# Performance work log

Measured on AMD Instinct MI355X. Metric: run time of the kernel, lower is better.

The kernel has to match this reference:

```python
import jax, jax.numpy as jnp
import numpy as np


def _run_stacked_lstm(x, init_hc, params):
    """x: [B,T,E]; init_hc: tuple of (h,c) per layer; params: tuple of (W,U,b) per layer.
    Keras LSTMCell gate order: i, f, g(candidate), o; sigmoid recurrent act, tanh act."""
    def step(carry, xt):
        inp = xt
        new = []
        for (h, c), (W, U, b) in zip(carry, params):
            z = inp @ W + h @ U + b                      # [B, 4*units]
            i, f, g, o = jnp.split(z, 4, axis=-1)
            c2 = jax.nn.sigmoid(f) * c + jax.nn.sigmoid(i) * jnp.tanh(g)
            h2 = jax.nn.sigmoid(o) * jnp.tanh(c2)
            new.append((h2, c2))
            inp = h2                                     # feed to next layer
        return tuple(new), inp
    carry, ys = jax.lax.scan(step, init_hc, jnp.swapaxes(x, 0, 1))
    return jnp.swapaxes(ys, 0, 1), carry                 # [B,T,units], final states


def setup_inputs() -> dict:
    key = jax.random.key(0)
    ks = jax.random.split(key, 20)
    B, T, V, E, H, L = 16, 64, 32000, 512, 512, 2
    s = 0.02
    inp = {
        'ids_1': jax.random.randint(ks[0], (B, T), 0, V),
        'ids_2': jax.random.randint(ks[1], (B, T), 0, V),
        'init_state': jax.random.normal(ks[2], (L, B, H), jnp.float32),
        'emb': jax.random.normal(ks[3], (V, E), jnp.float32) * s,
        'W1_0': jax.random.normal(ks[4], (E, 4 * H), jnp.float32) * s,
        'U1_0': jax.random.normal(ks[5], (H, 4 * H), jnp.float32) * s,
        'b1_0': jnp.zeros((4 * H,), jnp.float32),
        'W1_1': jax.random.normal(ks[6], (H, 4 * H), jnp.float32) * s,
        'U1_1': jax.random.normal(ks[7], (H, 4 * H), jnp.float32) * s,
        'b1_1': jnp.zeros((4 * H,), jnp.float32),
        'W2_0': jax.random.normal(ks[8], (E, 8 * H), jnp.float32) * s,
        'U2_0': jax.random.normal(ks[9], (2 * H, 8 * H), jnp.float32) * s,
        'b2_0': jnp.zeros((8 * H,), jnp.float32),
        'W2_1': jax.random.normal(ks[10], (2 * H, 8 * H), jnp.float32) * s,
        'U2_1': jax.random.normal(ks[11], (2 * H, 8 * H), jnp.float32) * s,
        'b2_1': jnp.zeros((8 * H,), jnp.float32),
        'Wp1': jax.random.normal(ks[12], (H, V), jnp.float32) * s,
        'bp1': jnp.zeros((V,), jnp.float32),
        'Wp2': jax.random.normal(ks[13], (2 * H, V), jnp.float32) * s,
        'bp2': jnp.zeros((V,), jnp.float32),
    }
    return inp


def reference(ids_1, ids_2, init_state, emb,
              W1_0, U1_0, b1_0, W1_1, U1_1, b1_1,
              W2_0, U2_0, b2_0, W2_1, U2_1, b2_1,
              Wp1, bp1, Wp2, bp2):
    L = init_state.shape[0]
    e1 = emb[ids_1]                                       # [B,T,E]
    e2 = emb[ids_2]
    # RNN1: initial (h,c) both set to init_state per layer
    init1 = tuple((init_state[l], init_state[l]) for l in range(L))
    p1 = ((W1_0, U1_0, b1_0), (W1_1, U1_1, b1_1))
    out1, st1 = _run_stacked_lstm(e1, init1, p1)
    logits1 = out1 @ Wp1 + bp1                            # [B,T,V]
    # RNN2: initial h = concat(init, h1_final), c = concat(init, c1_final)
    init2 = tuple((jnp.concatenate([init_state[l], st1[l][0]], axis=1),
                   jnp.concatenate([init_state[l], st1[l][1]], axis=1))
                  for l in range(L))
    p2 = ((W2_0, U2_0, b2_0), (W2_1, U2_1, b2_1))
    out2, _ = _run_stacked_lstm(e2, init2, p2)
    logits2 = out2 @ Wp2 + bp2                            # [B,T,V]
    return (logits1, logits2)
```

## Files before the change

### kernel.cpp

```cpp
#include <hip/hip_runtime.h>
#include <hip/hip_bf16.h>

#define B_ 16
#define T_ 64
#define E_ 512
#define H_ 512
#define V_ 32000

typedef __attribute__((ext_vector_type(4))) float f32x4;
typedef __attribute__((ext_vector_type(8))) short s16x8;

__device__ __forceinline__ float sigm(float x){ return 1.0f/(1.0f + __expf(-x)); }

__device__ __forceinline__ unsigned short f2bf(float x){
  unsigned int u = __float_as_uint(x);
  return (unsigned short)((u + 0x7FFFu + ((u>>16)&1u)) >> 16);
}

__device__ __forceinline__ unsigned load_coh(const unsigned* p){
  unsigned v;
  asm volatile("global_load_dword %0, %1, off sc0 sc1\n\ts_waitcnt vmcnt(0)"
               : "=v"(v) : "v"(p) : "memory");
  return v;
}
__device__ __forceinline__ void store_coh16(unsigned short* p, unsigned v){
  asm volatile("global_store_short %0, %1, off sc0 sc1" :: "v"(p), "v"(v) : "memory");
}
__device__ __forceinline__ void store_cohf(float* p, float v){
  asm volatile("global_store_dword %0, %1, off sc0 sc1" :: "v"(p), "v"(v) : "memory");
}
__device__ __forceinline__ void store_cohu(unsigned* p, unsigned v){
  asm volatile("global_store_dword %0, %1, off sc0 sc1" :: "v"(p), "v"(v) : "memory");
}

__device__ __forceinline__ void gbar3(unsigned* barb, unsigned bi1, int nblk,
                                      bool det, int myblk){
  asm volatile("s_waitcnt vmcnt(0)" ::: "memory");
  __syncthreads();
  const int tid = threadIdx.x;
  if(tid == 0) store_cohu(barb + (size_t)myblk*16, bi1);
  if(det){
    if(tid < nblk){
      const unsigned* fp = barb + (size_t)tid*16;
      while(load_coh(fp) < bi1) __builtin_amdgcn_s_sleep(1);
    }
    __syncthreads();
    if(tid < 8) store_cohu(barb + 4096 + (size_t)tid*16, bi1);
  } else {
    if(tid == 0){
      const unsigned* gp = barb + 4096 + (size_t)(myblk & 7)*16;
      while(load_coh(gp) < bi1) __builtin_amdgcn_s_sleep(1);
    }
  }
  __syncthreads();
}

__global__ void k_barinit(unsigned* bar){
  int i = blockIdx.x*256 + threadIdx.x;
  if(i < 16384) bar[i] = 0u;
}

__global__ void k_gather(const int* __restrict__ ids, const float* __restrict__ emb,
                         unsigned short* __restrict__ out){
  const int row = blockIdx.x;
  const int id  = ids[row];
  float4 v = *(const float4*)(emb + (size_t)id*E_ + threadIdx.x*4);
  ushort4 o;
  o.x = f2bf(v.x); o.y = f2bf(v.y); o.z = f2bf(v.z); o.w = f2bf(v.w);
  *(ushort4*)(out + (size_t)row*E_ + threadIdx.x*4) = o;
}

__device__ __forceinline__ void tcvt_dev(const float* __restrict__ in,
    unsigned short* __restrict__ out, int N, int Hp, int Kfull, int koff, int swz,
    int bx, int by, float (*tile)[33]){
  const int n0 = bx*32, k0 = by*32;
  const int x = threadIdx.x & 31, y = threadIdx.x >> 5;
  __syncthreads();
  #pragma unroll
  for(int i=0;i<4;i++){
    int k = y + i*8;
    tile[k][x] = in[(size_t)(k0+k)*N + n0 + x];
  }
  __syncthreads();
  #pragma unroll
  for(int i=0;i<4;i++){
    int nl = y + i*8;
    int n  = n0 + nl;
    int p  = Hp ? ((n % Hp)*4 + n / Hp) : n;
    int kk = koff + k0 + x;
    size_t idx;
    if(swz){
      int k2 = kk*2;
      int slot = ((k2>>4)&7) ^ (p&7);
      idx = (size_t)p*Kfull + (((k2 & ~127) | (slot<<4) | (k2 & 15)) >> 1);
    } else {
      idx = (size_t)p*Kfull + kk;
    }
    out[idx] = f2bf(tile[x][nl]);
  }
}

__global__ __launch_bounds__(256)
void k_tcvt(const float* __restrict__ in, unsigned short* __restrict__ out,
            int N, int Hp, int Kfull, int koff, int swz){
  __shared__ float tile[32][33];
  tcvt_dev(in, out, N, Hp, Kfull, koff, swz, blockIdx.x, blockIdx.y, tile);
}

__device__ __forceinline__ void tcvtw_dev(const float* __restrict__ in,
    unsigned short* __restrict__ out, int N, int K, int bx, int by,
    float (*tile)[257]){
  const int tid = threadIdx.x;
  const int n0 = bx*256, k0 = by*32;
  const int row = tid >> 3, nc = (tid & 7)*32;
  __syncthreads();
  #pragma unroll
  for(int j=0;j<8;j++){
    float4 v = *(const float4*)(in + (size_t)(k0+row)*N + n0 + nc + j*4);
    *(float4*)&tile[row][nc + j*4] = v;
  }
  __syncthreads();
  __align__(16) unsigned short vals[32];
  #pragma unroll
  for(int k=0;k<32;k++) vals[k] = f2bf(tile[k][tid]);
  unsigned short* op = out + (size_t)(n0+tid)*K + k0;
  #pragma unroll
  for(int j=0;j<4;j++)
    *(uint4*)(op + j*8) = *(const uint4*)&vals[j*8];
}

__global__ void k_bpack(const float* __restrict__ b, float* __restrict__ out, int H, int N){
  int p = blockIdx.x*256 + threadIdx.x;
  if(p < N) out[p] = b[(p&3)*H + (p>>2)];
}

__global__ void k_init1(const float* __restrict__ init_state,
                        unsigned short* h0i, float* c0i, unsigned short* h1i, float* c1i){
  int i = blockIdx.x*256 + threadIdx.x;
  if(i >= B_*H_) return;
  float v0 = init_state[i];
  float v1 = init_state[B_*H_ + i];
  h0i[i] = f2bf(v0); c0i[i] = v0;
  h1i[i] = f2bf(v1); c1i[i] = v1;
}

__global__ void k_init2(const float* __restrict__ init_state,
                        const unsigned short* __restrict__ h0seq1,
                        const unsigned short* __restrict__ h1seq1,
                        const float* __restrict__ c0f1, const float* __restrict__ c1f1,
                        unsigned short* h20i, unsigned short* h21i,
                        float* c20i, float* c21i){
  const int l = blockIdx.y;
  int i = blockIdx.x*256 + threadIdx.x;
  if(i >= B_*2*H_) return;
  const int r = i >> 10, j = i & 1023;
  unsigned short* ho = l ? h21i : h20i;
  float* co = l ? c21i : c20i;
  if(j < H_){
    float v = init_state[(size_t)l*B_*H_ + r*H_ + j];
    ho[i] = f2bf(v); co[i] = v;
  } else {
    const unsigned short* hs = l ? h1seq1 : h0seq1;
    const float* cf = l ? c1f1 : c0f1;
    ho[i] = hs[(size_t)((T_-1)*B_ + r)*H_ + (j - H_)];
    co[i] = cf[r*H_ + (j - H_)];
  }
}

__device__ __forceinline__ void mm_tile(const unsigned short* __restrict__ A,
    const unsigned short* __restrict__ Bt, const float* __restrict__ bias,
    float* __restrict__ C, int N, int K, int bm, int bn,
    unsigned short* As, unsigned short* Bs, int remap){
  const int tid = threadIdx.x;
  const int lane = tid & 63, w = tid >> 6;
  const int wm = (w>>1)*64, wn = (w&1)*64;
  const int l15 = lane & 15, kg = lane >> 4;
  f32x4 acc[4][4] = {};
  for(int k0=0; k0<K; k0+=64){
    __syncthreads();
    #pragma unroll
    for(int ch=0; ch<4; ch++){
      int off = ch*4096 + tid*16;
      int row = off >> 7;
      int s   = ((off >> 4) & 7) ^ (row & 7);
      __builtin_amdgcn_global_load_lds(
        (const __attribute__((address_space(1))) unsigned int*)(A + (size_t)(bm+row)*K + k0 + s*8),
        (__attribute__((address_space(3))) unsigned int*)((char*)As + off), 16, 0, 0);
    }
    #pragma unroll
    for(int ch=0; ch<4; ch++){
      int off = ch*4096 + tid*16;
      int row = off >> 7;
      int s   = ((off >> 4) & 7) ^ (row & 7);
      __builtin_amdgcn_global_load_lds(
        (const __attribute__((address_space(1))) unsigned int*)(Bt + (size_t)(bn+row)*K + k0 + s*8),
        (__attribute__((address_space(3))) unsigned int*)((char*)Bs + off), 16, 0, 0);
    }
    __syncthreads();
    #pragma unroll
    for(int q=0;q<2;q++){
      s16x8 af[4], bf[4];
      #pragma unroll
      for(int mt=0;mt<4;mt++){
        int row = wm + mt*16 + l15;
        int s = (q*4 + kg) ^ (row & 7);
        af[mt] = *(const s16x8*)(As + row*64 + s*8);
      }
      #pragma unroll
      for(int nt=0;nt<4;nt++){
        int row = wn + nt*16 + l15;
        int s = (q*4 + kg) ^ (row & 7);
        bf[nt] = *(const s16x8*)(Bs + row*64 + s*8);
      }
      #pragma unroll
      for(int mt=0;mt<4;mt++)
        #pragma unroll
        for(int nt=0;nt<4;nt++)
          acc[mt][nt] = __builtin_amdgcn_mfma_f32_16x16x32_bf16(af[mt], bf[nt], acc[mt][nt], 0, 0, 0);
    }
  }
  #pragma unroll
  for(int mt=0;mt<4;mt++){
    #pragma unroll
    for(int nt=0;nt<4;nt++){
      int col = bn + wn + nt*16 + l15;
      float bv = bias ? bias[col] : 0.f;
      #pragma unroll
      for(int e=0;e<4;e++){
        int row = bm + wm + mt*16 + kg*4 + e;
        int orow = remap ? ((row & 15)*T_ + (row >> 4)) : row;
        C[(size_t)orow*N + col] = acc[mt][nt][e] + bv;
      }
    }
  }
}

template<int BF32>
__global__ __launch_bounds__(256)
void k_mm(const unsigned short* __restrict__ A, const void* __restrict__ Bsrc,
          const float* __restrict__ bias, float* __restrict__ C,
          int M, int N, int K, int remap, int bm0){
  __shared__ __align__(16) unsigned short As[128*64];
  __shared__ __align__(16) unsigned short Bs[128*64];
  if(!BF32){
    mm_tile(A, (const unsigned short*)Bsrc, bias, C, N, K,
            bm0 + blockIdx.y*128, blockIdx.x*128, As, Bs, remap);
    return;
  }
  const int tid = threadIdx.x;
  const int lane = tid & 63, w = tid >> 6;
  const int wm = (w>>1)*64, wn = (w&1)*64;
  const int bm = bm0 + blockIdx.y*128, bn = blockIdx.x*128;
  const int l15 = lane & 15, kg = lane >> 4;
  f32x4 acc[4][4] = {};
  for(int k0=0; k0<K; k0+=64){
    __syncthreads();
    #pragma unroll
    for(int ch=0; ch<4; ch++){
      int off = ch*4096 + tid*16;
      int row = off >> 7;
      int s   = ((off >> 4) & 7) ^ (row & 7);
      __builtin_amdgcn_global_load_lds(
        (const __attribute__((address_space(1))) unsigned int*)(A + (size_t)(bm+row)*K + k0 + s*8),
        (__attribute__((address_space(3))) unsigned int*)((char*)As + off), 16, 0, 0);
    }
    {
      const float* Bf = (const float*)Bsrc;
      #pragma unroll
      for(int i=0;i<8;i++){
        int kl = (tid>>5) + i*8;
        int nl = (tid&31)*4;
        float4 v = *(const float4*)(Bf + (size_t)(k0+kl)*N + bn + nl);
        int slot = kl >> 3, kb = kl & 7;
        float vv[4] = {v.x, v.y, v.z, v.w};
        #pragma unroll
        for(int jj=0;jj<4;jj++){
          int n = nl + jj;
          Bs[n*64 + ((slot ^ (n&7))*8) + kb] = f2bf(vv[jj]);
        }
      }
    }
    __syncthreads();
    #pragma unroll
    for(int q=0;q<2;q++){
      s16x8 af[4], bf[4];
      #pragma unroll
      for(int mt=0;mt<4;mt++){
        int row = wm + mt*16 + l15;
        int s = (q*4 + kg) ^ (row & 7);
        af[mt] = *(const s16x8*)(As + row*64 + s*8);
      }
      #pragma unroll
      for(int nt=0;nt<4;nt++){
        int row = wn + nt*16 + l15;
        int s = (q*4 + kg) ^ (row & 7);
        bf[nt] = *(const s16x8*)(Bs + row*64 + s*8);
      }
      #pragma unroll
      for(int mt=0;mt<4;mt++)
        #pragma unroll
        for(int nt=0;nt<4;nt++)
          acc[mt][nt] = __builtin_amdgcn_mfma_f32_16x16x32_bf16(af[mt], bf[nt], acc[mt][nt], 0, 0, 0);
    }
  }
  #pragma unroll
  for(int mt=0;mt<4;mt++){
    #pragma unroll
    for(int nt=0;nt<4;nt++){
      int col = bn + wn + nt*16 + l15;
      float bv = bias ? bias[col] : 0.f;
      #pragma unroll
      for(int e=0;e<4;e++){
        int row = bm + wm + mt*16 + kg*4 + e;
        int orow = remap ? ((row & 15)*T_ + (row >> 4)) : row;
        C[(size_t)orow*N + col] = acc[mt][nt][e] + bv;
      }
    }
  }
}

template<int C, int K, int LAYER, int HU, int TB>
__device__ __forceinline__ void rnn_body(
    unsigned short* __restrict__ Uld, float* __restrict__ zp,
    const unsigned short* __restrict__ Uslice,
    const float* __restrict__ xw0, const float* __restrict__ bpk,
    const unsigned short* __restrict__ h0init, const unsigned short* __restrict__ h1init,
    const float* __restrict__ cinit,
    unsigned short* __restrict__ h0seq, unsigned short* __restrict__ h1seq,
    float* __restrict__ cfin, unsigned* bar, int cb, int nblk, bool det, int myblk)
{
  constexpr int KW = K/4, KS = KW/32, FR = C/16, UB = C/4;
  constexpr int K2 = K*2;
  constexpr int ITEMS = 16*UB;
  const int tid = threadIdx.x;
  const int lane = tid & 63, w = tid >> 6;
  const int l15 = lane & 15, kg = lane >> 4;

  constexpr int CP = (C*K2)/4096;
  #pragma unroll
  for(int i=0;i<CP;i++){
    __builtin_amdgcn_global_load_lds(
      (const __attribute__((address_space(1))) unsigned int*)((const char*)Uslice + i*4096 + tid*16),
      (__attribute__((address_space(3))) unsigned int*)((char*)Uld + i*4096 + tid*16), 16, 0, 0);
  }
  const int base_p = cb*C;
  const int base_u = cb*UB;
  float4 bvr = make_float4(0.f,0.f,0.f,0.f);
  int er = 0, eu = 0;
  if(tid < ITEMS){ er = tid / UB; eu = tid - er*UB; bvr = *(const float4*)(bpk + base_p + eu*4); }
  float creg = 0.f;
  unsigned short* hseqW = LAYER ? h1seq : h0seq;

  int cbyte[FR], cx[FR];
  #pragma unroll
  for(int f=0;f<FR;f++){ int c = f*16 + l15; cbyte[f] = c*K2; cx[f] = (c&7)<<4; }

  __syncthreads();

  for(int it = 0; it <= T_; ++it){
    const bool active = LAYER ? (it >= 1) : (it < T_);
    const int t = LAYER ? it-1 : it;
    if(active){
      const unsigned short* asrc;
      if constexpr(LAYER == 0){
        asrc = (t == 0) ? (h0init + l15*HU)
             : (h0seq + ((size_t)(TB ? ((t-1)*B_ + l15) : (l15*T_ + (t-1))))*HU);
      } else {
        if(w < 2){
          asrc = h0seq + ((size_t)(TB ? (t*B_ + l15) : (l15*T_ + t)))*HU;
        } else {
          asrc = ((t == 0) ? (h1init + l15*HU)
               : (h1seq + ((size_t)(TB ? ((t-1)*B_ + l15) : (l15*T_ + (t-1))))*HU)) - HU;
        }
      }
      f32x4 acc[FR];
      #pragma unroll
      for(int f=0;f<FR;f++) acc[f] = (f32x4){0.f,0.f,0.f,0.f};
      #pragma unroll
      for(int s=0;s<KS;s++){
        const int kel = w*KW + s*32 + kg*8;
        s16x8 a = *(const s16x8*)(asrc + kel);
        const int kb  = kel*2;
        const int kch = kb & ~127;
        const int ksl = (kb >> 4) & 7;
        #pragma unroll
        for(int f=0;f<FR;f++){
          const int ad = cbyte[f] + kch + ((ksl<<4) ^ cx[f]);
          s16x8 b = *(const s16x8*)((const char*)Uld + ad);
          acc[f] = __builtin_amdgcn_mfma_f32_16x16x32_bf16(a, b, acc[f], 0, 0, 0);
        }
      }
      #pragma unroll
      for(int f=0;f<FR;f++)
        #pragma unroll
        for(int e=0;e<4;e++)
          zp[(w*16 + kg*4 + e)*68 + f*16 + l15] = acc[f][e];
    }
    __syncthreads();
    if(active && tid < ITEMS){
      float4 z0 = *(const float4*)(zp + (     er)*68 + eu*4);
      float4 z1 = *(const float4*)(zp + (16 + er)*68 + eu*4);
      float4 z2 = *(const float4*)(zp + (32 + er)*68 + eu*4);
      float4 z3 = *(const float4*)(zp + (48 + er)*68 + eu*4);
      float si = z0.x+z1.x+z2.x+z3.x + bvr.x;
      float sf = z0.y+z1.y+z2.y+z3.y + bvr.y;
      float sg = z0.z+z1.z+z2.z+z3.z + bvr.z;
      float so = z0.w+z1.w+z2.w+z3.w + bvr.w;
      if constexpr(LAYER == 0){
        float4 xv = *(const float4*)(xw0 + ((size_t)(er*T_ + t))*(4*HU) + base_p + eu*4);
        si += xv.x; sf += xv.y; sg += xv.z; so += xv.w;
      }
      float cin = (t == 0) ? cinit[er*HU + base_u + eu] : creg;
      float c2 = sigm(sf)*cin + sigm(si)*tanhf(sg);
      float h2 = sigm(so)*tanhf(c2);
      creg = c2;
      size_t hrow = TB ? ((size_t)(t*B_ + er)) : ((size_t)(er*T_ + t));
      store_coh16(&hseqW[hrow*HU + base_u + eu], (unsigned)f2bf(h2));
      if(t == T_-1) store_cohf(&cfin[er*HU + base_u + eu], c2);
    }
    if(it < T_) gbar3(bar, (unsigned)(it+1), nblk, det, myblk);
  }
  asm volatile("s_waitcnt vmcnt(0)" ::: "memory");
  __syncthreads();
  if(tid == 0) store_cohu(bar + (size_t)myblk*16, (unsigned)(T_+1));
}

__global__ __launch_bounds__(256, 1)
void k_rnn1m(const unsigned short* __restrict__ Ut0, const unsigned short* __restrict__ WU1,
    const float* __restrict__ xw0, const float* __restrict__ bpk0, const float* __restrict__ bpk1,
    const unsigned short* __restrict__ h0init, const unsigned short* __restrict__ h1init,
    const float* __restrict__ c0init, const float* __restrict__ c1init,
    unsigned short* __restrict__ h0seq, unsigned short* __restrict__ h1seq,
    float* __restrict__ c0fin, float* __restrict__ c1fin, unsigned* bar,
    const int* __restrict__ ids2, const float* __restrict__ emb, unsigned short* __restrict__ ebuf2,
    const float* __restrict__ b2_0, const float* __restrict__ b2_1,
    float* __restrict__ bpk20, float* __restrict__ bpk21,
    const float* __restrict__ U2_0, unsigned short* __restrict__ ut0_2,
    const float* __restrict__ W2_0, unsigned short* __restrict__ wtmp2,
    const float* __restrict__ W2_1, const float* __restrict__ U2_1, unsigned short* __restrict__ wu1_2,
    const float* __restrict__ Wp1, unsigned short* __restrict__ wpT1,
    const float* __restrict__ Wp2, unsigned short* __restrict__ wpT2,
    const float* __restrict__ bp1, float* __restrict__ out1,
    float* __restrict__ xw2buf, int wide)
{
  constexpr int HU = 512, C0 = 64, C1 = 64;
  constexpr int NB0 = 4*HU/C0;
  constexpr int NRNN = NB0 + 4*HU/C1;
  constexpr int NS = 256 - NRNN;
  __shared__ __align__(16) unsigned short Uld[65536];
  __shared__ __align__(16) float zred[64*68];
  const int blk = blockIdx.x;
  const int tid = threadIdx.x;
  if(blk < NB0){
    rnn_body<C0, HU, 0, HU, 1>(Uld, zred, Ut0 + (size_t)blk*C0*HU, xw0, bpk0,
        h0init, h1init, c0init, h0seq, h1seq, c0fin, bar, blk, NRNN, blk==0, blk);
  } else if(blk < NRNN){
    rnn_body<C1, 2*HU, 1, HU, 1>(Uld, zred, WU1 + (size_t)(blk-NB0)*C1*2*HU, nullptr, bpk1,
        h0init, h1init, c1init, h0seq, h1seq, c1fin, bar, blk-NB0, NRNN, false, blk);
  } else {
    const int q = blk - NRNN;
    float (*tile)[33]   = (float(*)[33])Uld;
    float (*tile2)[257] = (float(*)[257])Uld;
    unsigned short* As = Uld;
    unsigned short* Bs = Uld + 8192;
    volatile int* rdy = (volatile int*)((char*)Uld + 128000);
    const int J0 = 512, J1 = J0+32, J2 = J1+4096, J3 = J2+2048, J4 = J3+4096, J5 = J4+4096;
    const int J6 = J5 + 2000;
    const int J7 = J6 + 4000;
    const int totJ = wide ? J7 : J5;
    for(int j = q; j < totJ; j += NS){
      if(j < J0){
        int row = j*2 + (tid>>7);
        int id = ids2[row];
        float4 v = *(const float4*)(emb + (size_t)id*E_ + (tid&127)*4);
        ushort4 o; o.x=f2bf(v.x); o.y=f2bf(v.y); o.z=f2bf(v.z); o.w=f2bf(v.w);
        *(ushort4*)(ebuf2 + (size_t)row*E_ + (tid&127)*4) = o;
      } else if(j < J1){
        int jj = j - J0;
        const float* b = (jj < 16) ? b2_0 : b2_1;
        float* o = (jj < 16) ? bpk20 : bpk21;
        int p = (jj & 15)*256 + tid;
        o[p] = b[(p&3)*1024 + (p>>2)];
      } else if(j < J2){
        int r = j - J1; tcvt_dev(U2_0, ut0_2, 4096, 1024, 1024, 0, 1, r%128, r/128, tile);
      } else if(j < J3){
        int r = j - J2; tcvt_dev(W2_0, wtmp2, 4096, 1024, 512, 0, 0, r%128, r/128, tile);
      } else if(j < J4){
        int r = j - J3; tcvt_dev(W2_1, wu1_2, 4096, 1024, 2048, 0, 1, r%128, r/128, tile);
      } else if(j < J5){
        int r = j - J4; tcvt_dev(U2_1, wu1_2, 4096, 1024, 2048, 1024, 1, r%128, r/128, tile);
      } else if(j < J6){
        int r = j - J5; tcvtw_dev(Wp1, wpT1, 32000, 512, r%125, r/125, tile2);
      } else {
        int r = j - J6; tcvtw_dev(Wp2, wpT2, 32000, 1024, r%125, r/125, tile2);
      }
    }
    if(!wide) return;
    __syncthreads();
    __threadfence();
    if(tid == 0)
      __hip_atomic_fetch_add(bar + 5120, 1u, __ATOMIC_RELAXED, __HIP_MEMORY_SCOPE_AGENT);
    if(tid == 0){
      while(load_coh(bar + 5120) < (unsigned)NS) __builtin_amdgcn_s_sleep(8);
    }
    __syncthreads();
    if(xw2buf){
      for(int t2 = q; t2 < 256; t2 += NS)
        mm_tile(ebuf2, wtmp2, nullptr, xw2buf, 4096, 512, (t2>>5)*128, (t2&31)*128, As, Bs, 0);
    }
    for(int g = 0; g < 8; ++g){
      const unsigned req = 8u*(unsigned)g + 9u;
      for(;;){
        if(tid == 0) *rdy = 1;
        __syncthreads();
        if(tid < 32){
          if(load_coh(bar + (size_t)(NB0 + tid)*16) < req) *rdy = 0;
        }
        __syncthreads();
        if(*rdy) break;
        __builtin_amdgcn_s_sleep(16);
      }
      for(int n = q; n < 250; n += NS)
        mm_tile(h1seq, wpT1, bp1, out1, V_, 512, g*128, n*128, As, Bs, 1);
    }
  }
}

__global__ __launch_bounds__(256, 1)
void k_rnn2m(const unsigned short* __restrict__ Ut0, const unsigned short* __restrict__ WU1,
    const float* __restrict__ xw0, const float* __restrict__ bpk0, const float* __restrict__ bpk1,
    const unsigned short* __restrict__ h0init, const unsigned short* __restrict__ h1init,
    const float* __restrict__ c0init, const float* __restrict__ c1init,
    unsigned short* __restrict__ h0seq, unsigned short* __restrict__ h1seq,
    float* __restrict__ c0fin, float* __restrict__ c1fin, unsigned* bar,
    const unsigned short* __restrict__ wpT2,
    const float* __restrict__ bp2, float* __restrict__ out2, int wide)
{
  constexpr int HU = 1024, C0 = 64, C1 = 32;
  constexpr int NB0 = 4*HU/C0;
  constexpr int NRNN = NB0 + 4*HU/C1;
  constexpr int NS = 64;
  __shared__ __align__(16) unsigned short Uld[65536];
  __shared__ __align__(16) float zred[64*68];
  const int blk = blockIdx.x;
  const int tid = threadIdx.x;
  if(blk < NB0){
    rnn_body<C0, HU, 0, HU, 1>(Uld, zred, Ut0 + (size_t)blk*C0*HU, xw0, bpk0,
        h0init, h1init, c0init, h0seq, h1seq, c0fin, bar, blk, NRNN, blk==0, blk);
  } else if(blk < NRNN){
    rnn_body<C1, 2*HU, 1, HU, 1>(Uld, zred, WU1 + (size_t)(blk-NB0)*C1*2*HU, nullptr, bpk1,
        h0init, h1init, c1init, h0seq, h1seq, c1fin, bar, blk-NB0, NRNN, false, blk);
  } else if(wide){
    const int q = blk - NRNN;
    unsigned short* As = Uld;
    unsigned short* Bs = Uld + 8192;
    volatile int* rdy = (volatile int*)((char*)Uld + 128000);
    for(int g = 0; g < 6; ++g){
      const unsigned req = 8u*(unsigned)g + 9u;
      for(;;){
        if(tid == 0) *rdy = 1;
        __syncthreads();
        if(tid < 128){
          if(load_coh(bar + (size_t)(NB0 + tid)*16) < req) *rdy = 0;
        }
        __syncthreads();
        if(*rdy) break;
        __builtin_amdgcn_s_sleep(16);
      }
      for(int n = q; n < 250; n += NS)
        mm_tile(h1seq, wpT2, bp2, out2, V_, 1024, g*128, n*128, As, Bs, 1);
    }
  }
}

extern "C" void kernel_launch(void* const* d_in, const int* in_sizes, int n_in,
                              void* d_out, int out_size, void* d_ws, size_t ws_size,
                              hipStream_t stream){
  const int*   ids1 = (const int*)d_in[0];
  const int*   ids2 = (const int*)d_in[1];
  const float* init = (const float*)d_in[2];
  const float* emb  = (const float*)d_in[3];
  const float* W1_0 = (const float*)d_in[4];
  const float* U1_0 = (const float*)d_in[5];
  const float* b1_0 = (const float*)d_in[6];
  const float* W1_1 = (const float*)d_in[7];
  const float* U1_1 = (const float*)d_in[8];
  const float* b1_1 = (const float*)d_in[9];
  const float* W2_0 = (const float*)d_in[10];
  const float* U2_0 = (const float*)d_in[11];
  const float* b2_0 = (const float*)d_in[12];
  const float* W2_1 = (const float*)d_in[13];
  const float* U2_1 = (const float*)d_in[14];
  const float* b2_1 = (const float*)d_in[15];
  const float* Wp1  = (const float*)d_in[16];
  const float* bp1  = (const float*)d_in[17];
  const float* Wp2  = (const float*)d_in[18];
  const float* bp2  = (const float*)d_in[19];
  float* out1 = (float*)d_out;
  float* out2 = out1 + (size_t)B_*T_*V_;

  char* base = (char*)d_ws;
  float*          xw    = (float*)(base);
  unsigned short* ut0_1 = (unsigned short*)(base + (16u<<20));
  unsigned short* wu1_1 = (unsigned short*)(base + (18u<<20));
  unsigned short* ut0_2 = (unsigned short*)(base + (22u<<20));
  unsigned short* wu1_2 = (unsigned short*)(base + (30u<<20));
  unsigned short* wtmp  = (unsigned short*)(base + (46u<<20));
  unsigned short* ebuf  = (unsigned short*)(base + (50u<<20));
  unsigned short* h0s1  = (unsigned short*)(base + (51u<<20));
  unsigned short* h1s1  = (unsigned short*)(base + (52u<<20));
  unsigned short* h0s2  = (unsigned short*)(base + (53u<<20));
  unsigned short* h1s2  = (unsigned short*)(base + (55u<<20));
  char* M = base + (57u<<20);
  unsigned short* h0i1 = (unsigned short*)(M);
  unsigned short* h1i1 = (unsigned short*)(M + 16384);
  float* c0i1 = (float*)(M + 32768);
  float* c1i1 = (float*)(M + 65536);
  unsigned short* h2i0 = (unsigned short*)(M + 98304);
  unsigned short* h2i1 = (unsigned short*)(M + 131072);
  float* c2i0 = (float*)(M + 163840);
  float* c2i1 = (float*)(M + 229376);
  float* c0f1 = (float*)(M + 294912);
  float* c1f1 = (float*)(M + 327680);
  float* c0f2 = (float*)(M + 360448);
  float* c1f2 = (float*)(M + 425984);
  float* bpk10 = (float*)(M + 491520);
  float* bpk11 = (float*)(M + 499712);
  float* bpk20 = (float*)(M + 507904);
  float* bpk21 = (float*)(M + 524288);
  unsigned* bar1 = (unsigned*)(M + 540672);
  unsigned* bar2 = (unsigned*)(M + 540672 + 32768);
  unsigned short* wpT1 = (unsigned short*)(base + (58u<<20));
  unsigned short* wpT2 = (unsigned short*)(base + (90u<<20));
  float*          xw2  = (float*)(base + (153u<<20));
  const size_t NEED_W  = ((size_t)90u<<20) + (size_t)V_*1024*2;
  const size_t NEED_W2 = ((size_t)169u<<20);
  const bool wide  = ws_size >= NEED_W;
  const bool wide2 = ws_size >= NEED_W2;
  float* xw2p = wide2 ? xw2 : xw;

  k_barinit<<<dim3(64), dim3(256), 0, stream>>>(bar1);

  k_init1<<<dim3(32), dim3(256), 0, stream>>>(init, h0i1, c0i1, h1i1, c1i1);
  k_gather<<<dim3(B_*T_), dim3(128), 0, stream>>>(ids1, emb, ebuf);
  k_tcvt<<<dim3(64, 16), dim3(256), 0, stream>>>(U1_0, ut0_1, 2048, 512, 512, 0, 1);
  k_tcvt<<<dim3(64, 16), dim3(256), 0, stream>>>(W1_0, wtmp,  2048, 512, 512, 0, 0);
  k_tcvt<<<dim3(64, 16), dim3(256), 0, stream>>>(W1_1, wu1_1, 2048, 512, 1024, 0, 1);
  k_tcvt<<<dim3(64, 16), dim3(256), 0, stream>>>(U1_1, wu1_1, 2048, 512, 1024, 512, 1);
  k_bpack<<<dim3(8),  dim3(256), 0, stream>>>(b1_0, bpk10, 512, 2048);
  k_bpack<<<dim3(8),  dim3(256), 0, stream>>>(b1_1, bpk11, 512, 2048);
  k_mm<0><<<dim3(16, 8), dim3(256), 0, stream>>>(ebuf, wtmp, nullptr, xw, 1024, 2048, 512, 0, 0);

  k_rnn1m<<<dim3(256), dim3(256), 0, stream>>>(ut0_1, wu1_1, xw, bpk10, bpk11,
      h0i1, h1i1, c0i1, c1i1, h0s1, h1s1, c0f1, c1f1, bar1,
      ids2, emb, ebuf, b2_0, b2_1, bpk20, bpk21,
      U2_0, ut0_2, W2_0, wtmp, W2_1, U2_1, wu1_2,
      Wp1, wpT1, Wp2, wpT2, bp1, out1,
      (wide && wide2) ? xw2 : nullptr, (int)wide);

  if(!wide){
    k_mm<1><<<dim3(250, 8), dim3(256), 0, stream>>>(h1s1, Wp1, bp1, out1, 1024, V_, 512, 1, 0);
  }
  if(!wide || !wide2){
    k_mm<0><<<dim3(32, 8), dim3(256), 0, stream>>>(ebuf, wtmp, nullptr, xw, 1024, 4096, 512, 0, 0);
  }
  k_init2<<<dim3(64, 2), dim3(256), 0, stream>>>(init, h0s1, h1s1, c0f1, c1f1,
                                                 h2i0, h2i1, c2i0, c2i1);

  k_rnn2m<<<dim3(256), dim3(256), 0, stream>>>(ut0_2, wu1_2, xw2p, bpk20, bpk21,
      h2i0, h2i1, c2i0, c2i1, h0s2, h1s2, c0f2, c1f2, bar2,
      wpT2, bp2, out2, (int)wide);

  if(wide){
    k_mm<0><<<dim3(250, 2), dim3(256), 0, stream>>>(h1s2, wpT2, bp2, out2, 1024, V_, 1024, 1, 768);
  } else {
    k_mm<1><<<dim3(250, 8), dim3(256), 0, stream>>>(h1s2, Wp2, bp2, out2, 1024, V_, 1024, 1, 0);
  }
}
```

Before: 1.029 ms.

## Remove overlapped projection from RNN2 kernel and run full projection afterwards

Drops the 64 extra blocks in the second RNN kernel that computed the vocab projection for the first 768 rows while the recurrence ran, leaving a 192-block recurrence-only kernel. The full 1024-row projection for logits2 is now done by a separate matmul launch afterwards. This removes the polling and contention of the projection blocks against the latency-bound recurrence, but gives up the overlap, so most of the projection work now sits on the critical path.

```diff
diff --git a/kernel.cpp b/kernel.cpp
--- a/kernel.cpp
+++ b/kernel.cpp
@@ -526,51 +526,28 @@
   }
 }
 
+template<int HU, int C0, int C1>
 __global__ __launch_bounds__(256, 1)
-void k_rnn2m(const unsigned short* __restrict__ Ut0, const unsigned short* __restrict__ WU1,
-    const float* __restrict__ xw0, const float* __restrict__ bpk0, const float* __restrict__ bpk1,
-    const unsigned short* __restrict__ h0init, const unsigned short* __restrict__ h1init,
-    const float* __restrict__ c0init, const float* __restrict__ c1init,
-    unsigned short* __restrict__ h0seq, unsigned short* __restrict__ h1seq,
-    float* __restrict__ c0fin, float* __restrict__ c1fin, unsigned* bar,
-    const unsigned short* __restrict__ wpT2,
-    const float* __restrict__ bp2, float* __restrict__ out2, int wide)
+void k_rnn(const unsigned short* __restrict__ Ut0, const unsigned short* __restrict__ WU1,
+           const float* __restrict__ xw0, const float* __restrict__ bpk0, const float* __restrict__ bpk1,
+           const unsigned short* __restrict__ h0init, const unsigned short* __restrict__ h1init,
+           const float* __restrict__ c0init, const float* __restrict__ c1init,
+           unsigned short* __restrict__ h0seq, unsigned short* __restrict__ h1seq,
+           float* __restrict__ c0fin, float* __restrict__ c1fin, unsigned* bar)
 {
-  constexpr int HU = 1024, C0 = 64, C1 = 32;
   constexpr int NB0 = 4*HU/C0;
-  constexpr int NRNN = NB0 + 4*HU/C1;
-  constexpr int NS = 64;
-  __shared__ __align__(16) unsigned short Uld[65536];
+  constexpr int UMAXE = (C0*HU > C1*2*HU) ? C0*HU : C1*2*HU;
+  __shared__ __align__(16) unsigned short Uld[UMAXE];
   __shared__ __align__(16) float zred[64*68];
+  const int nblk = gridDim.x;
+  const bool det = (blockIdx.x == 0);
   const int blk = blockIdx.x;
-  const int tid = threadIdx.x;
-  if(blk < NB0){
+  if(blk < NB0)
     rnn_body<C0, HU, 0, HU, 1>(Uld, zred, Ut0 + (size_t)blk*C0*HU, xw0, bpk0,
-        h0init, h1init, c0init, h0seq, h1seq, c0fin, bar, blk, NRNN, blk==0, blk);
-  } else if(blk < NRNN){
+                               h0init, h1init, c0init, h0seq, h1seq, c0fin, bar, blk, nblk, det, blk);
+  else
     rnn_body<C1, 2*HU, 1, HU, 1>(Uld, zred, WU1 + (size_t)(blk-NB0)*C1*2*HU, nullptr, bpk1,
-        h0init, h1init, c1init, h0seq, h1seq, c1fin, bar, blk-NB0, NRNN, false, blk);
-  } else if(wide){
-    const int q = blk - NRNN;
-    unsigned short* As = Uld;
-    unsigned short* Bs = Uld + 8192;
-    volatile int* rdy = (volatile int*)((char*)Uld + 128000);
-    for(int g = 0; g < 6; ++g){
-      const unsigned req = 8u*(unsigned)g + 9u;
-      for(;;){
-        if(tid == 0) *rdy = 1;
-        __syncthreads();
-        if(tid < 128){
-          if(load_coh(bar + (size_t)(NB0 + tid)*16) < req) *rdy = 0;
-        }
-        __syncthreads();
-        if(*rdy) break;
-        __builtin_amdgcn_s_sleep(16);
-      }
-      for(int n = q; n < 250; n += NS)
-        mm_tile(h1seq, wpT2, bp2, out2, V_, 1024, g*128, n*128, As, Bs, 1);
-    }
-  }
+                               h0init, h1init, c1init, h0seq, h1seq, c1fin, bar, blk-NB0, nblk, det, blk);
 }
 
 extern "C" void kernel_launch(void* const* d_in, const int* in_sizes, int n_in,
@@ -637,7 +614,7 @@
   const size_t NEED_W2 = ((size_t)169u<<20);
   const bool wide  = ws_size >= NEED_W;
   const bool wide2 = ws_size >= NEED_W2;
-  float* xw2p = wide2 ? xw2 : xw;
+  float* xw2p = (wide && wide2) ? xw2 : xw;
 
   k_barinit<<<dim3(64), dim3(256), 0, stream>>>(bar1);
 
@@ -667,12 +644,11 @@
   k_init2<<<dim3(64, 2), dim3(256), 0, stream>>>(init, h0s1, h1s1, c0f1, c1f1,
                                                  h2i0, h2i1, c2i0, c2i1);
 
-  k_rnn2m<<<dim3(256), dim3(256), 0, stream>>>(ut0_2, wu1_2, xw2p, bpk20, bpk21,
-      h2i0, h2i1, c2i0, c2i1, h0s2, h1s2, c0f2, c1f2, bar2,
-      wpT2, bp2, out2, (int)wide);
+  k_rnn<1024, 64, 32><<<dim3(192), dim3(256), 0, stream>>>(ut0_2, wu1_2, xw2p, bpk20, bpk21,
+      h2i0, h2i1, c2i0, c2i1, h0s2, h1s2, c0f2, c1f2, bar2);
 
   if(wide){
-    k_mm<0><<<dim3(250, 2), dim3(256), 0, stream>>>(h1s2, wpT2, bp2, out2, 1024, V_, 1024, 1, 768);
+    k_mm<0><<<dim3(250, 8), dim3(256), 0, stream>>>(h1s2, wpT2, bp2, out2, 1024, V_, 1024, 1, 0);
   } else {
     k_mm<1><<<dim3(250, 8), dim3(256), 0, stream>>>(h1s2, Wp2, bp2, out2, 1024, V_, 1024, 1, 0);
   }
```

After: 892.5 us. 1.15x faster.
